# Kernel optimization log

Measured on AMD Instinct MI355X. Metric: run time of the kernel, lower is better.

The kernel has to match this reference:

```python
import jax, jax.numpy as jnp
import numpy as np

NEG_INF = -1e9


def setup_inputs() -> dict:
    key = jax.random.key(0)
    k1, k2, k3, k4, k5, k6 = jax.random.split(key, 6)
    B, P, N, C, H = 32, 512, 64, 9, 128
    polylines = jax.random.normal(k1, (B, P, N, C), dtype=jnp.float32)
    polylines_mask = jax.random.uniform(k2, (B, P, N)) > 0.1
    # MLP params (Linear(C,H) -> ReLU -> Linear(H,H)), torch-style init scale
    W1 = jax.random.uniform(k3, (C, H), minval=-1.0, maxval=1.0) / jnp.sqrt(C)
    b1 = jax.random.uniform(k4, (H,), minval=-1.0, maxval=1.0) / jnp.sqrt(C)
    W2 = jax.random.uniform(k5, (H, H), minval=-1.0, maxval=1.0) / jnp.sqrt(H)
    b2 = jax.random.uniform(k6, (H,), minval=-1.0, maxval=1.0) / jnp.sqrt(H)
    return {"polylines": polylines, "polylines_mask": polylines_mask,
            "W1": W1, "b1": b1, "W2": W2, "b2": b2}


def reference(polylines, polylines_mask, W1, b1, W2, b2):
    # Point MLP applied to all points (invalid ones are overwritten below,
    # identical math to the torch masked-gather version).
    h = jax.nn.relu(jnp.einsum('bpnc,ch->bpnh', polylines, W1) + b1)
    feat = jnp.einsum('bpnh,hd->bpnd', h, W2) + b2  # [B,P,N,H]
    feat = jnp.where(polylines_mask[..., None], feat, NEG_INF)
    pooled = jnp.max(feat, axis=2)  # [B,P,H]
    # Polylines with no valid points pooled to NEG_INF -> zero them out.
    any_valid = jnp.any(polylines_mask, axis=2)  # [B,P]
    return jnp.where(any_valid[..., None], pooled, 0.0)
```

## Files before the change

kernel.cpp:

```cpp
#include <hip/hip_runtime.h>


using bf16x8 = __attribute__((ext_vector_type(8))) short;
using f32x4  = __attribute__((ext_vector_type(4))) float;

#define MFMA32(A,B,C) __builtin_amdgcn_mfma_f32_16x16x32_bf16((A),(B),(C),0,0,0)

__device__ __forceinline__ f32x4 vmax4(f32x4 a, f32x4 b) {
  return __builtin_elementwise_max(a, b);
}

__device__ __forceinline__ unsigned short f2bf(float f) {
  union { float f; unsigned int u; } v; v.f = f;
  unsigned int r = v.u + 0x7fffu + ((v.u >> 16) & 1u);
  return (unsigned short)(r >> 16);
}

__device__ __forceinline__ unsigned int pack_bf2(float a, float b) {
  union { float f; unsigned int u; } ua, ub; ua.f = a; ub.f = b;
  return __builtin_amdgcn_perm(ub.u + 0x8000u, ua.u + 0x8000u, 0x07060302u);
}

__global__ void prep1(const float* __restrict__ W1, const float* __restrict__ W2,
                      const void* __restrict__ mask,
                      unsigned short* __restrict__ w1sw, unsigned short* __restrict__ w2sw,
                      int* __restrict__ flag) {
  int b = blockIdx.x, t = threadIdx.x;
  if (b == 0) {
    __shared__ int cnt;
    if (t == 0) cnt = 0;
    __syncthreads();
    const unsigned char* mb = (const unsigned char*)mask;
    int local = 0;
    for (int i = t * 16; i < t * 16 + 16; i++) local += (mb[i] != 0) ? 1 : 0;
    atomicAdd(&cnt, local);
    __syncthreads();
    if (t == 0) *flag = (cnt > 2800) ? 1 : 0;
  } else if (b <= 2) {
    int e = (b - 1) * 256 + t;
    int lane = e & 63, grp = e >> 6;
    int li = lane & 15, q = lane >> 4;
    int h = grp * 16 + li;
    int c0 = q * 8;
    #pragma unroll
    for (int j = 0; j < 8; j++) {
      int c = c0 + j;
      w1sw[e * 8 + j] = f2bf((c < 9) ? W1[c * 128 + h] : 0.f);
    }
  } else {
    int e = (b - 3) * 256 + t;
    if (e < 2048) {
      int lane = e & 63, grp = e >> 6;
      int wr = grp >> 4, sub = grp & 15;
      int ks = sub >> 2, td = sub & 3;
      int li = lane & 15, q = lane >> 4;
      int d = wr * 64 + td * 16 + li;
      int h0 = ks * 32 + q * 8;
      #pragma unroll
      for (int j = 0; j < 8; j++)
        w2sw[e * 8 + j] = f2bf(W2[(h0 + j) * 128 + d]);
    }
  }
}

__global__ __launch_bounds__(256, 4) void poly_main_k(
    const float* __restrict__ X, const void* __restrict__ mask,
    const float* __restrict__ b1g, const float* __restrict__ b2g,
    const unsigned short* __restrict__ w1sw, const unsigned short* __restrict__ w2sw,
    const int* __restrict__ flagp, float* __restrict__ out)
{
  __shared__ __align__(16) unsigned char smem[32768];
  float*          Xs = (float*)smem;
  unsigned short* Hb = (unsigned short*)smem;
  float*          P  = (float*)smem;

  const int tid  = threadIdx.x;
  const int lane = tid & 63;
  const int w    = tid >> 6;
  const int wr   = w >> 1, wc = w & 1;
  const int li   = lane & 15, q = lane >> 4;

  float mf[4];
  {
    int flag = *flagp;
    long long mb = (long long)blockIdx.x * 128 + wc * 64 + li;
    if (flag) {
      const unsigned char* mp = (const unsigned char*)mask;
      #pragma unroll
      for (int tm = 0; tm < 4; tm++) mf[tm] = mp[mb + tm * 16] ? 0.f : -4e9f;
    } else {
      const int* mp = (const int*)mask;
      #pragma unroll
      for (int tm = 0; tm < 4; tm++) mf[tm] = mp[mb + tm * 16] ? 0.f : -4e9f;
    }
  }

  {
    const f32x4* xg = (const f32x4*)(X + (long long)blockIdx.x * 1152);
    f32x4* xl = (f32x4*)Xs;
    xl[tid] = xg[tid];
    if (tid < 32) xl[tid + 256] = xg[tid + 256];
  }
  __syncthreads();

  bf16x8 bx[4];
  #pragma unroll
  for (int tm = 0; tm < 4; tm++) {
    int m = wc * 64 + tm * 16 + li;
    const float* xr = Xs + m * 9;
    union { bf16x8 v; unsigned int u[4]; } uu;
    uu.u[0] = uu.u[1] = uu.u[2] = uu.u[3] = 0u;
    if (q == 0) {
      uu.u[0] = pack_bf2(xr[0], xr[1]); uu.u[1] = pack_bf2(xr[2], xr[3]);
      uu.u[2] = pack_bf2(xr[4], xr[5]); uu.u[3] = pack_bf2(xr[6], xr[7]);
    } else if (q == 1) {
      uu.u[0] = pack_bf2(xr[8], 0.f);
    }
    bx[tm] = uu.v;
  }
  __syncthreads();

  #pragma unroll
  for (int th = 0; th < 4; th++) {
    bf16x8 a1 = *(const bf16x8*)(w1sw + ((wr * 4 + th) * 64 + lane) * 8);
    f32x4 bv = *(const f32x4*)(b1g + wr * 64 + th * 16 + q * 4);
    f32x4 acc[4];
    #pragma unroll
    for (int tm = 0; tm < 4; tm++) acc[tm] = bv;
    #pragma unroll
    for (int tm = 0; tm < 4; tm++) acc[tm] = MFMA32(a1, bx[tm], acc[tm]);
    #pragma unroll
    for (int tm = 0; tm < 4; tm++) {
      int m = wc * 64 + tm * 16 + li;
      f32x4 v = vmax4(acc[tm], f32x4{0.f, 0.f, 0.f, 0.f});
      uint2 hv;
      hv.x = pack_bf2(v[0], v[1]);
      hv.y = pack_bf2(v[2], v[3]);
      int chunk = (wr * 8 + th * 2 + (q >> 1)) ^ li;
      *(uint2*)(Hb + m * 128 + chunk * 8 + (q & 1) * 4) = hv;
    }
  }
  __syncthreads();

  f32x4 pooled[4];
  #pragma unroll
  for (int tm = 0; tm < 4; tm++) {
    int m = wc * 64 + tm * 16 + li;
    f32x4 acc[4];
    #pragma unroll
    for (int td = 0; td < 4; td++) acc[td] = f32x4{0.f, 0.f, 0.f, 0.f};
    #pragma unroll
    for (int ks = 0; ks < 4; ks++) {
      int chunk = (ks * 4 + q) ^ li;
      bf16x8 bb = *(const bf16x8*)(Hb + m * 128 + chunk * 8);
      #pragma unroll
      for (int td = 0; td < 4; td++) {
        bf16x8 a2 = *(const bf16x8*)(w2sw + (((wr * 16 + ks * 4 + td) * 64) + lane) * 8);
        acc[td] = MFMA32(a2, bb, acc[td]);
      }
    }
    if (tm == 0) {
      #pragma unroll
      for (int td = 0; td < 4; td++) pooled[td] = acc[td] + mf[0];
    } else {
      #pragma unroll
      for (int td = 0; td < 4; td++) pooled[td] = vmax4(pooled[td], acc[td] + mf[tm]);
    }
  }
  #pragma unroll
  for (int td = 0; td < 4; td++)
    pooled[td] += *(const f32x4*)(b2g + wr * 64 + td * 16 + q * 4);

  __syncthreads();
  #pragma unroll
  for (int td = 0; td < 4; td++)
    *(f32x4*)(P + (wc * 16 + li) * 132 + wr * 64 + td * 16 + q * 4) = pooled[td];
  __syncthreads();

  {
    int p = tid >> 7, d = tid & 127;
    const float* Pp = P + p * (16 * 132) + d;
    float v = Pp[0];
    #pragma unroll
    for (int j = 1; j < 16; j++) v = fmaxf(v, Pp[j * 132]);
    if (v < -1e8f) v = 0.f;
    out[(long long)blockIdx.x * 256 + tid] = v;
  }
}

extern "C" void kernel_launch(void* const* d_in, const int* in_sizes, int n_in,
                              void* d_out, int out_size, void* d_ws, size_t ws_size,
                              hipStream_t stream) {
  const float* X    = (const float*)d_in[0];
  const void*  mask = d_in[1];
  const float* W1   = (const float*)d_in[2];
  const float* b1   = (const float*)d_in[3];
  const float* W2   = (const float*)d_in[4];
  const float* b2   = (const float*)d_in[5];
  float* out = (float*)d_out;

  unsigned short* w1sw = (unsigned short*)d_ws;
  unsigned short* w2sw = (unsigned short*)((char*)d_ws + 8192);
  int* flag            = (int*)((char*)d_ws + 40960);

  prep1<<<11, 256, 0, stream>>>(W1, W2, mask, w1sw, w2sw, flag);
  poly_main_k<<<8192, 256, 0, stream>>>(X, mask, b1, b2, w1sw, w2sw, flag, out);
}
```

Baseline: 141.1 us.

## Halve block size, stage inputs via direct global-to-LDS loads, use hardware bf16 pack

Each block now covers one polyline (64 points) with 128 threads instead of two polylines with 256, which cuts LDS per block and doubles the grid. Input rows are copied straight from global memory into LDS with global_load_lds, so they no longer pass through registers. The second barrier goes away because Xs now sits in its own region apart from Hb. The software bf16 packing is replaced by the v_cvt_pk_bf16_f32 instruction, and s_setprio is raised around the MFMA bursts. The trade-off is more blocks, each with less work, so the per-block prologue and the W1/W2 fragment loads repeat more often.

```diff
diff --git a/kernel.cpp b/kernel.cpp
--- a/kernel.cpp
+++ b/kernel.cpp
@@ -16,9 +16,10 @@
   return (unsigned short)(r >> 16);
 }
 
-__device__ __forceinline__ unsigned int pack_bf2(float a, float b) {
-  union { float f; unsigned int u; } ua, ub; ua.f = a; ub.f = b;
-  return __builtin_amdgcn_perm(ub.u + 0x8000u, ua.u + 0x8000u, 0x07060302u);
+__device__ __forceinline__ unsigned int pk2(float a, float b) {
+  unsigned int r;
+  asm("v_cvt_pk_bf16_f32 %0, %1, %2" : "=v"(r) : "v"(a), "v"(b));
+  return r;
 }
 
 __global__ void prep1(const float* __restrict__ W1, const float* __restrict__ W2,
@@ -63,27 +64,40 @@
   }
 }
 
-__global__ __launch_bounds__(256, 4) void poly_main_k(
+__global__ __launch_bounds__(128, 4) void poly_main_k(
     const float* __restrict__ X, const void* __restrict__ mask,
     const float* __restrict__ b1g, const float* __restrict__ b2g,
     const unsigned short* __restrict__ w1sw, const unsigned short* __restrict__ w2sw,
     const int* __restrict__ flagp, float* __restrict__ out)
 {
-  __shared__ __align__(16) unsigned char smem[32768];
-  float*          Xs = (float*)smem;
+  __shared__ __align__(16) unsigned char smem[18688];
   unsigned short* Hb = (unsigned short*)smem;
   float*          P  = (float*)smem;
+  float*          Xs = (float*)(smem + 16384);
 
   const int tid  = threadIdx.x;
   const int lane = tid & 63;
-  const int w    = tid >> 6;
-  const int wr   = w >> 1, wc = w & 1;
+  const int wr   = tid >> 6;
   const int li   = lane & 15, q = lane >> 4;
+
+  {
+    const char* xg = (const char*)X + (long long)blockIdx.x * 2304;
+    unsigned ldsoff = (unsigned)(tid & 64) * 16;
+    __builtin_amdgcn_global_load_lds(
+        (const __attribute__((address_space(1))) unsigned int*)(xg + tid * 16),
+        (__attribute__((address_space(3))) unsigned int*)((char*)Xs + ldsoff),
+        16, 0, 0);
+    if (tid < 16)
+      __builtin_amdgcn_global_load_lds(
+          (const __attribute__((address_space(1))) unsigned int*)(xg + 2048 + tid * 16),
+          (__attribute__((address_space(3))) unsigned int*)((char*)Xs + 2048),
+          16, 0, 0);
+  }
 
   float mf[4];
   {
     int flag = *flagp;
-    long long mb = (long long)blockIdx.x * 128 + wc * 64 + li;
+    long long mb = (long long)blockIdx.x * 64 + li;
     if (flag) {
       const unsigned char* mp = (const unsigned char*)mask;
       #pragma unroll
@@ -95,30 +109,22 @@
     }
   }
 
-  {
-    const f32x4* xg = (const f32x4*)(X + (long long)blockIdx.x * 1152);
-    f32x4* xl = (f32x4*)Xs;
-    xl[tid] = xg[tid];
-    if (tid < 32) xl[tid + 256] = xg[tid + 256];
-  }
   __syncthreads();
 
   bf16x8 bx[4];
   #pragma unroll
   for (int tm = 0; tm < 4; tm++) {
-    int m = wc * 64 + tm * 16 + li;
-    const float* xr = Xs + m * 9;
+    const float* xr = Xs + (tm * 16 + li) * 9;
     union { bf16x8 v; unsigned int u[4]; } uu;
     uu.u[0] = uu.u[1] = uu.u[2] = uu.u[3] = 0u;
     if (q == 0) {
-      uu.u[0] = pack_bf2(xr[0], xr[1]); uu.u[1] = pack_bf2(xr[2], xr[3]);
-      uu.u[2] = pack_bf2(xr[4], xr[5]); uu.u[3] = pack_bf2(xr[6], xr[7]);
+      uu.u[0] = pk2(xr[0], xr[1]); uu.u[1] = pk2(xr[2], xr[3]);
+      uu.u[2] = pk2(xr[4], xr[5]); uu.u[3] = pk2(xr[6], xr[7]);
     } else if (q == 1) {
-      uu.u[0] = pack_bf2(xr[8], 0.f);
+      uu.u[0] = pk2(xr[8], 0.f);
     }
     bx[tm] = uu.v;
   }
-  __syncthreads();
 
   #pragma unroll
   for (int th = 0; th < 4; th++) {
@@ -127,15 +133,17 @@
     f32x4 acc[4];
     #pragma unroll
     for (int tm = 0; tm < 4; tm++) acc[tm] = bv;
+    __builtin_amdgcn_s_setprio(1);
     #pragma unroll
     for (int tm = 0; tm < 4; tm++) acc[tm] = MFMA32(a1, bx[tm], acc[tm]);
+    __builtin_amdgcn_s_setprio(0);
     #pragma unroll
     for (int tm = 0; tm < 4; tm++) {
-      int m = wc * 64 + tm * 16 + li;
+      int m = tm * 16 + li;
       f32x4 v = vmax4(acc[tm], f32x4{0.f, 0.f, 0.f, 0.f});
       uint2 hv;
-      hv.x = pack_bf2(v[0], v[1]);
-      hv.y = pack_bf2(v[2], v[3]);
+      hv.x = pk2(v[0], v[1]);
+      hv.y = pk2(v[2], v[3]);
       int chunk = (wr * 8 + th * 2 + (q >> 1)) ^ li;
       *(uint2*)(Hb + m * 128 + chunk * 8 + (q & 1) * 4) = hv;
     }
@@ -145,7 +153,7 @@
   f32x4 pooled[4];
   #pragma unroll
   for (int tm = 0; tm < 4; tm++) {
-    int m = wc * 64 + tm * 16 + li;
+    int m = tm * 16 + li;
     f32x4 acc[4];
     #pragma unroll
     for (int td = 0; td < 4; td++) acc[td] = f32x4{0.f, 0.f, 0.f, 0.f};
@@ -153,11 +161,13 @@
     for (int ks = 0; ks < 4; ks++) {
       int chunk = (ks * 4 + q) ^ li;
       bf16x8 bb = *(const bf16x8*)(Hb + m * 128 + chunk * 8);
+      __builtin_amdgcn_s_setprio(1);
       #pragma unroll
       for (int td = 0; td < 4; td++) {
         bf16x8 a2 = *(const bf16x8*)(w2sw + (((wr * 16 + ks * 4 + td) * 64) + lane) * 8);
         acc[td] = MFMA32(a2, bb, acc[td]);
       }
+      __builtin_amdgcn_s_setprio(0);
     }
     if (tm == 0) {
       #pragma unroll
@@ -174,17 +184,16 @@
   __syncthreads();
   #pragma unroll
   for (int td = 0; td < 4; td++)
-    *(f32x4*)(P + (wc * 16 + li) * 132 + wr * 64 + td * 16 + q * 4) = pooled[td];
+    *(f32x4*)(P + li * 132 + wr * 64 + td * 16 + q * 4) = pooled[td];
   __syncthreads();
 
   {
-    int p = tid >> 7, d = tid & 127;
-    const float* Pp = P + p * (16 * 132) + d;
+    const float* Pp = P + tid;
     float v = Pp[0];
     #pragma unroll
     for (int j = 1; j < 16; j++) v = fmaxf(v, Pp[j * 132]);
     if (v < -1e8f) v = 0.f;
-    out[(long long)blockIdx.x * 256 + tid] = v;
+    out[(long long)blockIdx.x * 128 + tid] = v;
   }
 }
 
@@ -204,5 +213,5 @@
   int* flag            = (int*)((char*)d_ws + 40960);
 
   prep1<<<11, 256, 0, stream>>>(W1, W2, mask, w1sw, w2sw, flag);
-  poly_main_k<<<8192, 256, 0, stream>>>(X, mask, b1, b2, w1sw, w2sw, flag, out);
-}
+  poly_main_k<<<16384, 128, 0, stream>>>(X, mask, b1, b2, w1sw, w2sw, flag, out);
+}
```

New measurement: 161.2 us. 14.2% more time.
